# Kernel tuning notes

Hardware: AMD Instinct MI355X
Metric: run time of the kernel (lower is better)

Reference implementation:

```python
import jax, jax.numpy as jnp
import numpy as np

N, D, H, E, K = 4096, 256, 1024, 8, 2  # tokens, hid_dim, expert hidden, n_experts, topk


def setup_inputs() -> dict:
    key = jax.random.key(0)
    ks = jax.random.split(key, 5)
    s = 0.02
    return {
        "x": jax.random.normal(ks[0], (N, D), jnp.float32),
        "gate_W": jax.random.normal(ks[1], (E, D), jnp.float32) * s,  # nn.Linear(hid_dim, n_exp).weight
        "gate_b": jnp.zeros((E,), jnp.float32),
        "W1": jax.random.normal(ks[2], (E, D, H), jnp.float32) * s,   # per-expert FFN layer 1
        "b1": jnp.zeros((E, H), jnp.float32),
        "W2": jax.random.normal(ks[3], (E, H, D), jnp.float32) * s,   # per-expert FFN layer 2
        "b2": jnp.zeros((E, D), jnp.float32),
        "temperature": jnp.array(1.0, jnp.float32),
    }


def reference(x, gate_W, gate_b, W1, b1, W2, b2, temperature):
    # forward() unsqueezes 2D input to [N, 1, D]
    x3 = x[:, None, :]                                           # [N,1,D]
    # _router: gate linear over last dim, squeeze L=1
    gate_scores = (jnp.einsum('nld,ed->nle', x3, gate_W) + gate_b)[:, 0, :]  # [N,E]
    gate_scores = gate_scores / temperature                      # router_act='lambda' -> identity
    _, topk_idx = jax.lax.top_k(gate_scores, K)                  # [N,K]

    # _moe_batch_forward: repeat_interleave tokens K times, route slot s to expert topk_idx.flat[s]
    xs = jnp.repeat(x3, K, axis=0)                               # [N*K,1,D]
    eid = topk_idx.reshape(-1)                                   # [N*K] int
    out = jnp.zeros((N * K, 1, D), x.dtype)
    for e in range(E):  # small fixed expert loop; masks partition the slots
        h = jax.nn.relu(jnp.einsum('sld,dh->slh', xs, W1[e]) + b1[e])  # [N*K,1,H]
        y = jnp.einsum('slh,hd->sld', h, W2[e]) + b2[e]                # [N*K,1,D]
        out = out + jnp.where((eid == e)[:, None, None], y, 0.0)
    out = out.reshape(N, K, 1, D)
    # gatter='sum': sum over the K expert slots -> [N,1,D]
    return out.sum(axis=1)
```

## Files before the change

### kernel.cpp

```cpp
#include <hip/hip_runtime.h>
#include <hip/hip_bf16.h>
#include <stdint.h>

#define NTOK 4096
#define DIM  256
#define HID  1024
#define NEXP 8
#define MTILE 32
#define HC 32
#define HSLICE 512
#define NSLICE 2
#define NCHUNK (HSLICE / HC)

typedef float f32x4 __attribute__((ext_vector_type(4)));
typedef short s16x8 __attribute__((ext_vector_type(8)));

__device__ __forceinline__ unsigned short f2bf(float f) {
  union { float f; unsigned u; } v; v.f = f;
  unsigned r = v.u + 0x7FFFu + ((v.u >> 16) & 1u);
  return (unsigned short)(r >> 16);
}
__device__ __forceinline__ float bf2f(unsigned short s) {
  union { float f; unsigned u; } v; v.u = ((unsigned)s) << 16;
  return v.f;
}
__device__ __forceinline__ void mfma16(f32x4& acc, s16x8 a, s16x8 b) {
  asm("v_mfma_f32_16x16x32_bf16 %0, %1, %2, %0" : "+v"(acc) : "v"(a), "v"(b));
}
__device__ __forceinline__ void accfence(f32x4& a) {
  asm volatile("s_nop 7" : "+v"(a));
}
__device__ __forceinline__ void initfence(f32x4& a) {
  asm volatile("s_nop 1" : "+v"(a));
}

__global__ __launch_bounds__(256) void prep(const float* __restrict__ W1,
                                            const float* __restrict__ W2,
                                            unsigned short* __restrict__ W1T,
                                            unsigned short* __restrict__ W2T,
                                            int* __restrict__ counts) {
  __shared__ float tile[32][33];
  int id = blockIdx.x;
  int tx = threadIdx.x, ty = threadIdx.y;
  if (id == 0 && ty == 0 && tx < NEXP) counts[tx] = 0;

  const float* in; unsigned short* out; int R, C, bx, by, e, sw;
  if (id < 2048) {
    e = id >> 8; int rem = id & 255; by = rem >> 5; bx = rem & 31;
    in = W1; out = W1T; R = 256; C = 1024; sw = 1;
  } else {
    int id2 = id - 2048;
    e = id2 >> 8; int rem = id2 & 255; by = (rem >> 3) & 31; bx = rem & 7;
    in = W2; out = W2T; R = 1024; C = 256; sw = 0;
  }
  int r0 = by * 32, c0 = bx * 32;
  const float* ip = in + (size_t)e * R * C;
  unsigned short* op = out + (size_t)e * R * C;
  #pragma unroll
  for (int k = 0; k < 4; ++k)
    tile[ty + 8*k][tx] = ip[(size_t)(r0 + ty + 8*k) * C + c0 + tx];
  __syncthreads();
  #pragma unroll
  for (int k = 0; k < 4; ++k) {
    float v = tile[tx][ty + 8*k];
    if (sw) {
      int row = c0 + ty + 8*k;
      int col = r0 + tx;
      op[(size_t)row * R + (col ^ ((row & 7) << 3))] = f2bf(v);
    } else {
      int d = c0 + ty + 8*k;
      int h = r0 + tx;
      int ch = h >> 5, kk = h & 31;
      int slot = (kk >> 3) ^ ((d >> 1) & 3);
      op[(size_t)ch * (DIM * 32) + d * 32 + slot * 8 + (kk & 7)] = f2bf(v);
    }
  }
}

__global__ __launch_bounds__(256) void gate_route(const float* __restrict__ x,
    const float* __restrict__ gW, const float* __restrict__ gb,
    const float* __restrict__ temp,
    int* __restrict__ counts, int* __restrict__ list,
    unsigned short* __restrict__ xbf) {
  __shared__ int pairs[16][2];
  __shared__ int lcnt[NEXP], lbase[NEXP], lrank[NEXP];
  int tid = threadIdx.x;
  int w = tid >> 6, lane = tid & 63;
  int sl = lane & 15, g = lane >> 4;
  if (tid < NEXP) { lcnt[tid] = 0; lrank[tid] = 0; }
  __syncthreads();
  int t0 = blockIdx.x * 16;
  int tok = w * 4 + g;
  int n = t0 + tok;

  float4 xv[4];
  #pragma unroll
  for (int p = 0; p < 4; ++p)
    xv[p] = *reinterpret_cast<const float4*>(x + (size_t)n * DIM + sl * 16 + p * 4);
  {
    s16x8 xb0, xb1;
    xb0[0]=(short)f2bf(xv[0].x); xb0[1]=(short)f2bf(xv[0].y); xb0[2]=(short)f2bf(xv[0].z); xb0[3]=(short)f2bf(xv[0].w);
    xb0[4]=(short)f2bf(xv[1].x); xb0[5]=(short)f2bf(xv[1].y); xb0[6]=(short)f2bf(xv[1].z); xb0[7]=(short)f2bf(xv[1].w);
    xb1[0]=(short)f2bf(xv[2].x); xb1[1]=(short)f2bf(xv[2].y); xb1[2]=(short)f2bf(xv[2].z); xb1[3]=(short)f2bf(xv[2].w);
    xb1[4]=(short)f2bf(xv[3].x); xb1[5]=(short)f2bf(xv[3].y); xb1[6]=(short)f2bf(xv[3].z); xb1[7]=(short)f2bf(xv[3].w);
    *reinterpret_cast<s16x8*>(xbf + (size_t)n * DIM + sl * 16)     = xb0;
    *reinterpret_cast<s16x8*>(xbf + (size_t)n * DIM + sl * 16 + 8) = xb1;
  }
  float acc[NEXP];
  #pragma unroll
  for (int e = 0; e < NEXP; ++e) {
    const float* we = gW + (size_t)e * DIM + sl * 16;
    float a = 0.f;
    #pragma unroll
    for (int p = 0; p < 4; ++p) {
      float4 wv = *reinterpret_cast<const float4*>(we + p * 4);
      a += xv[p].x*wv.x + xv[p].y*wv.y + xv[p].z*wv.z + xv[p].w*wv.w;
    }
    acc[e] = a;
  }
  #pragma unroll
  for (int off = 1; off < 16; off <<= 1) {
    #pragma unroll
    for (int e = 0; e < NEXP; ++e) acc[e] += __shfl_xor(acc[e], off);
  }
  if (sl == 0) {
    float t = temp[0];
    float s[NEXP];
    #pragma unroll
    for (int e = 0; e < NEXP; ++e) s[e] = (acc[e] + gb[e]) / t;
    int b0 = 0; float v0 = s[0];
    #pragma unroll
    for (int e = 1; e < NEXP; ++e) if (s[e] > v0) { v0 = s[e]; b0 = e; }
    int b1i = 0; float v1 = -3.4e38f;
    #pragma unroll
    for (int e = 0; e < NEXP; ++e) if (e != b0 && s[e] > v1) { v1 = s[e]; b1i = e; }
    pairs[tok][0] = b0;
    pairs[tok][1] = b1i;
    atomicAdd(&lcnt[b0], 1);
    atomicAdd(&lcnt[b1i], 1);
  }
  __syncthreads();
  if (tid < NEXP) lbase[tid] = atomicAdd(&counts[tid], lcnt[tid]);
  __syncthreads();
  if (tid < 32) {
    int tk = tid >> 1;
    int e = pairs[tk][tid & 1];
    int r = atomicAdd(&lrank[e], 1);
    list[e * NTOK + lbase[e] + r] = (t0 + tk) * 2 + (tid & 1);
  }
}

__global__ __launch_bounds__(256, 2) void moe_ffn(
    const unsigned short* __restrict__ xbf,
    const unsigned short* __restrict__ W1T,
    const unsigned short* __restrict__ W2T,
    const float* __restrict__ b1g, const float* __restrict__ b2g,
    const int* __restrict__ counts, const int* __restrict__ list,
    unsigned short* __restrict__ ybuf) {
  int b = blockIdx.x;
  int e = b & 7;
  int r = b >> 3;
  int s = r & (NSLICE - 1);
  int t = r >> 1;
  int cnt = counts[e];
  if (t * MTILE >= cnt) return;

  __shared__ __align__(16) short W1b[2][HC * 256];
  __shared__ __align__(16) short W2b[2][256 * HC];
  __shared__ __align__(16) short hs[2][32][40];
  __shared__ float b1s[HSLICE];

  int tid = threadIdx.x;
  int l = tid & 63, w = tid >> 6;
  int lr = l & 15, lg = l >> 4, kg = lg * 8;
  int wm = w & 1, wn = w >> 1;
  int hbase = s * HSLICE;
  const int* mylist = list + e * NTOK + t * MTILE;
  const unsigned short* W1e = W1T + (size_t)e * HID * DIM;
  const unsigned short* W2e = W2T + (size_t)e * HID * DIM;

  auto stage = [&](int hc, int buf) {
    const char* src1 = (const char*)(W1e + (size_t)hc * DIM);
    char* dst1 = (char*)&W1b[buf][0];
    const char* src2 = (const char*)(W2e + (size_t)(hc >> 5) * (DIM * 32));
    char* dst2 = (char*)&W2b[buf][0];
    #pragma unroll
    for (int i = 0; i < 4; ++i) {
      int off = w * 4096 + i * 1024;
      __builtin_amdgcn_global_load_lds(
        (const __attribute__((address_space(1))) void*)(src1 + off + l * 16),
        (__attribute__((address_space(3))) void*)(dst1 + off), 16, 0, 0);
      __builtin_amdgcn_global_load_lds(
        (const __attribute__((address_space(1))) void*)(src2 + off + l * 16),
        (__attribute__((address_space(3))) void*)(dst2 + off), 16, 0, 0);
    }
  };

  stage(hbase, 0);
  for (int i = tid; i < HSLICE; i += 256) b1s[i] = b1g[e * HID + hbase + i];

  s16x8 xa[8];
  {
    int row = wm * 16 + lr;
    int grow = t * MTILE + row;
    int entry = (grow < cnt) ? mylist[row] : mylist[0];
    const unsigned short* xsrc = xbf + (size_t)(entry >> 1) * DIM;
    #pragma unroll
    for (int kb = 0; kb < 8; ++kb)
      xa[kb] = *(const s16x8*)(xsrc + kb * 32 + kg);
  }

  f32x4 acc[8] = {};
  #pragma unroll
  for (int n = 0; n < 8; ++n) initfence(acc[n]);

  __syncthreads();

  int swz = (lr & 7) << 3;
  int brow = (wn * 16 + lr) << 8;

  #pragma unroll 2
  for (int c = 0; c < NCHUNK; ++c) {
    int buf = c & 1;

    asm volatile("s_waitcnt vmcnt(0)" ::: "memory");
    __builtin_amdgcn_s_barrier();
    __builtin_amdgcn_sched_barrier(0);

    if (c + 1 < NCHUNK) stage(hbase + (c + 1) * HC, buf ^ 1);

    f32x4 h0 = {}, h1 = {};
    initfence(h0); initfence(h1);
    const short* w1p = &W1b[buf][0];
    #pragma unroll
    for (int kb = 0; kb < 8; ++kb) {
      s16x8 bv = *(const s16x8*)&w1p[brow + ((kb * 32 + kg) ^ swz)];
      if (kb & 1) mfma16(h1, xa[kb], bv); else mfma16(h0, xa[kb], bv);
    }
    accfence(h0); accfence(h1);
    h0 += h1;
    float bb = b1s[c * HC + wn * 16 + lr];
    #pragma unroll
    for (int q = 0; q < 4; ++q)
      hs[buf][wm * 16 + lg * 4 + q][wn * 16 + lr] = (short)f2bf(fmaxf(h0[q] + bb, 0.f));

    asm volatile("s_waitcnt lgkmcnt(0)" ::: "memory");
    __builtin_amdgcn_s_barrier();
    __builtin_amdgcn_sched_barrier(0);

    {
      s16x8 a0 = *(const s16x8*)&hs[buf][wm * 16 + lr][kg];
      const short* w2p = &W2b[buf][0];
      #pragma unroll
      for (int n = 0; n < 8; ++n) {
        int d = wn * 128 + n * 16 + lr;
        s16x8 bv = *(const s16x8*)&w2p[(d << 5) + ((lg ^ ((d >> 1) & 3)) << 3)];
        mfma16(acc[n], a0, bv);
      }
    }
  }

  #pragma unroll
  for (int n = 0; n < 8; ++n) accfence(acc[n]);
  float b2v[8];
  #pragma unroll
  for (int n = 0; n < 8; ++n) b2v[n] = (s == 0) ? b2g[e * DIM + wn * 128 + n * 16 + lr] : 0.f;
  #pragma unroll
  for (int q = 0; q < 4; ++q) {
    int lrow = wm * 16 + lg * 4 + q;
    int grow = t * MTILE + lrow;
    if (grow < cnt) {
      int entry = mylist[lrow];
      unsigned short* yrow = ybuf + ((size_t)entry * NSLICE + s) * DIM + wn * 128 + lr;
      #pragma unroll
      for (int n = 0; n < 8; ++n)
        yrow[n * 16] = f2bf(acc[n][q] + b2v[n]);
    }
  }
}

__global__ __launch_bounds__(256) void reduce4(const unsigned short* __restrict__ yb,
                                               float* __restrict__ out) {
  int i = (blockIdx.x * 256 + threadIdx.x) * 8;
  int n = i >> 8, d = i & 255;
  const unsigned short* base = yb + ((size_t)n * 4) * DIM + d;
  float sum[8] = {0,0,0,0,0,0,0,0};
  #pragma unroll
  for (int r = 0; r < 4; ++r) {
    s16x8 v = *(const s16x8*)(base + r * DIM);
    #pragma unroll
    for (int j = 0; j < 8; ++j) sum[j] += bf2f((unsigned short)v[j]);
  }
  float4 o0 = {sum[0], sum[1], sum[2], sum[3]};
  float4 o1 = {sum[4], sum[5], sum[6], sum[7]};
  *(float4*)(out + i) = o0;
  *(float4*)(out + i + 4) = o1;
}

extern "C" void kernel_launch(void* const* d_in, const int* in_sizes, int n_in,
                              void* d_out, int out_size, void* d_ws, size_t ws_size,
                              hipStream_t stream) {
  const float* x    = (const float*)d_in[0];
  const float* gW   = (const float*)d_in[1];
  const float* gb   = (const float*)d_in[2];
  const float* W1   = (const float*)d_in[3];
  const float* b1   = (const float*)d_in[4];
  const float* W2   = (const float*)d_in[5];
  const float* b2   = (const float*)d_in[6];
  const float* temp = (const float*)d_in[7];
  float* out = (float*)d_out;

  char* ws = (char*)d_ws;
  int*            counts = (int*)(ws + 0);
  int*            list   = (int*)(ws + 256);
  unsigned short* xbf    = (unsigned short*)(ws + 131584);
  unsigned short* W1T    = (unsigned short*)(ws + 2228736);
  unsigned short* W2T    = (unsigned short*)(ws + 6423040);
  unsigned short* ybuf   = (unsigned short*)(ws + 10617344);

  prep<<<4096, dim3(32, 8, 1), 0, stream>>>(W1, W2, W1T, W2T, counts);
  gate_route<<<NTOK/16, 256, 0, stream>>>(x, gW, gb, temp, counts, list, xbf);
  moe_ffn<<<NEXP * (NTOK/MTILE) * NSLICE, 256, 0, stream>>>(xbf, W1T, W2T, b1, b2, counts, list, ybuf);
  reduce4<<<NTOK*DIM/2048, 256, 0, stream>>>(ybuf, out);
}
```

Baseline: 61.14 us.

## Skew second GEMM by one chunk and split weight staging for deeper pipelining

The loop is restructured so each chunk's W2 MFMA work uses the hidden activations from the previous chunk. This cuts the loop to one barrier per iteration instead of two. W1 and W2 staging are split: W1 is prefetched one chunk ahead and W2 is loaded for the current chunk, with a partial vmcnt wait so the newest loads stay in flight. The b1 bias moves from LDS into registers and the loop is fully unrolled. The risks are possible cross-wave visibility gaps for async global-to-LDS loads, since there is no full vmcnt wait before the barrier, plus a wasted wrap-around W1 load on the last iteration and higher register pressure.

```diff
diff --git a/kernel.cpp b/kernel.cpp
--- a/kernel.cpp
+++ b/kernel.cpp
@@ -168,7 +168,6 @@
   __shared__ __align__(16) short W1b[2][HC * 256];
   __shared__ __align__(16) short W2b[2][256 * HC];
   __shared__ __align__(16) short hs[2][32][40];
-  __shared__ float b1s[HSLICE];
 
   int tid = threadIdx.x;
   int l = tid & 63, w = tid >> 6;
@@ -179,25 +178,35 @@
   const unsigned short* W1e = W1T + (size_t)e * HID * DIM;
   const unsigned short* W2e = W2T + (size_t)e * HID * DIM;
 
-  auto stage = [&](int hc, int buf) {
-    const char* src1 = (const char*)(W1e + (size_t)hc * DIM);
-    char* dst1 = (char*)&W1b[buf][0];
-    const char* src2 = (const char*)(W2e + (size_t)(hc >> 5) * (DIM * 32));
-    char* dst2 = (char*)&W2b[buf][0];
+  auto stage1 = [&](int hc, int buf) {
+    const char* src = (const char*)(W1e + (size_t)hc * DIM);
+    char* dst = (char*)&W1b[buf][0];
     #pragma unroll
     for (int i = 0; i < 4; ++i) {
       int off = w * 4096 + i * 1024;
       __builtin_amdgcn_global_load_lds(
-        (const __attribute__((address_space(1))) void*)(src1 + off + l * 16),
-        (__attribute__((address_space(3))) void*)(dst1 + off), 16, 0, 0);
+        (const __attribute__((address_space(1))) void*)(src + off + l * 16),
+        (__attribute__((address_space(3))) void*)(dst + off), 16, 0, 0);
+    }
+  };
+  auto stage2 = [&](int hc, int buf) {
+    const char* src = (const char*)(W2e + (size_t)(hc >> 5) * (DIM * 32));
+    char* dst = (char*)&W2b[buf][0];
+    #pragma unroll
+    for (int i = 0; i < 4; ++i) {
+      int off = w * 4096 + i * 1024;
       __builtin_amdgcn_global_load_lds(
-        (const __attribute__((address_space(1))) void*)(src2 + off + l * 16),
-        (__attribute__((address_space(3))) void*)(dst2 + off), 16, 0, 0);
+        (const __attribute__((address_space(1))) void*)(src + off + l * 16),
+        (__attribute__((address_space(3))) void*)(dst + off), 16, 0, 0);
     }
   };
 
-  stage(hbase, 0);
-  for (int i = tid; i < HSLICE; i += 256) b1s[i] = b1g[e * HID + hbase + i];
+  stage1(hbase, 0);
+
+  float bbreg[NCHUNK];
+  #pragma unroll
+  for (int c = 0; c < NCHUNK; ++c)
+    bbreg[c] = b1g[e * HID + hbase + c * HC + wn * 16 + lr];
 
   s16x8 xa[8];
   {
@@ -219,44 +228,60 @@
   int swz = (lr & 7) << 3;
   int brow = (wn * 16 + lr) << 8;
 
-  #pragma unroll 2
+  #pragma unroll
   for (int c = 0; c < NCHUNK; ++c) {
-    int buf = c & 1;
-
-    asm volatile("s_waitcnt vmcnt(0)" ::: "memory");
+    int P = c & 1, Q = P ^ 1;
+
+    asm volatile("s_waitcnt lgkmcnt(0)" ::: "memory");
     __builtin_amdgcn_s_barrier();
     __builtin_amdgcn_sched_barrier(0);
 
-    if (c + 1 < NCHUNK) stage(hbase + (c + 1) * HC, buf ^ 1);
+    stage1(hbase + (((c + 1) & (NCHUNK - 1)) * HC), Q);
+    stage2(hbase + c * HC, P);
+
+    asm volatile("s_waitcnt vmcnt(8)" ::: "memory");
+    __builtin_amdgcn_sched_barrier(0);
 
     f32x4 h0 = {}, h1 = {};
     initfence(h0); initfence(h1);
-    const short* w1p = &W1b[buf][0];
+    const short* w1p = &W1b[P][0];
     #pragma unroll
     for (int kb = 0; kb < 8; ++kb) {
       s16x8 bv = *(const s16x8*)&w1p[brow + ((kb * 32 + kg) ^ swz)];
       if (kb & 1) mfma16(h1, xa[kb], bv); else mfma16(h0, xa[kb], bv);
     }
-    accfence(h0); accfence(h1);
-    h0 += h1;
-    float bb = b1s[c * HC + wn * 16 + lr];
-    #pragma unroll
-    for (int q = 0; q < 4; ++q)
-      hs[buf][wm * 16 + lg * 4 + q][wn * 16 + lr] = (short)f2bf(fmaxf(h0[q] + bb, 0.f));
-
-    asm volatile("s_waitcnt lgkmcnt(0)" ::: "memory");
-    __builtin_amdgcn_s_barrier();
-    __builtin_amdgcn_sched_barrier(0);
-
-    {
-      s16x8 a0 = *(const s16x8*)&hs[buf][wm * 16 + lr][kg];
-      const short* w2p = &W2b[buf][0];
+
+    if (c > 0) {
+      s16x8 a0 = *(const s16x8*)&hs[Q][wm * 16 + lr][kg];
+      const short* w2p = &W2b[Q][0];
       #pragma unroll
       for (int n = 0; n < 8; ++n) {
         int d = wn * 128 + n * 16 + lr;
         s16x8 bv = *(const s16x8*)&w2p[(d << 5) + ((lg ^ ((d >> 1) & 3)) << 3)];
         mfma16(acc[n], a0, bv);
       }
+    }
+
+    accfence(h0); accfence(h1);
+    h0 += h1;
+    float bb = bbreg[c];
+    #pragma unroll
+    for (int q = 0; q < 4; ++q)
+      hs[P][wm * 16 + lg * 4 + q][wn * 16 + lr] = (short)f2bf(fmaxf(h0[q] + bb, 0.f));
+  }
+
+  asm volatile("s_waitcnt vmcnt(0) lgkmcnt(0)" ::: "memory");
+  __builtin_amdgcn_s_barrier();
+  __builtin_amdgcn_sched_barrier(0);
+  {
+    const int Q = (NCHUNK - 1) & 1;
+    s16x8 a0 = *(const s16x8*)&hs[Q][wm * 16 + lr][kg];
+    const short* w2p = &W2b[Q][0];
+    #pragma unroll
+    for (int n = 0; n < 8; ++n) {
+      int d = wn * 128 + n * 16 + lr;
+      s16x8 bv = *(const s16x8*)&w2p[(d << 5) + ((lg ^ ((d >> 1) & 3)) << 3)];
+      mfma16(acc[n], a0, bv);
     }
   }
 
```

Result: faster. 56.23 us (-8.0%).
